# Kernel tuning notes

Hardware: AMD Instinct MI355X
Metric: run time of the kernel (lower is better)

## Reference

```python
import math
import jax, jax.numpy as jnp
import numpy as np

B, T, C = 2, 2048, 2048
NQ, NKV, H = 16, 4, 128
EPS = 1e-6
ROPE_BASE = 5.0e6


def setup_inputs() -> dict:
    key = jax.random.key(0)
    ks = jax.random.split(key, 6)
    x = jax.random.normal(ks[0], (B, T, C), dtype=jnp.float32)
    s = 0.02
    Wq = jax.random.normal(ks[1], (C, NQ * H), dtype=jnp.float32) * s
    Wk = jax.random.normal(ks[2], (C, NKV * H), dtype=jnp.float32) * s
    Wv = jax.random.normal(ks[3], (C, NKV * H), dtype=jnp.float32) * s
    Wo = jax.random.normal(ks[4], (NQ * H, C), dtype=jnp.float32) * s
    q_norm_w = jnp.ones((H,), dtype=jnp.float32)
    k_norm_w = jnp.ones((H,), dtype=jnp.float32)
    # RoPE tables (seq_start = 0)
    inv_freq = 1.0 / (ROPE_BASE ** (jnp.arange(0, H, 2, dtype=jnp.float32) / H))
    t = jnp.arange(T, dtype=jnp.float32)
    freqs = jnp.einsum('i,j->ij', t, inv_freq)          # [T, H/2]
    emb = jnp.concatenate([freqs, freqs], axis=-1)       # [T, H]
    cos = jnp.cos(emb)
    sin = jnp.sin(emb)
    # additive causal mask (finite large negative to stay nan-free)
    causal = jnp.tril(jnp.ones((T, T), dtype=bool))
    attn_mask = jnp.where(causal, 0.0, -1e9).astype(jnp.float32)
    return {"x": x, "Wq": Wq, "Wk": Wk, "Wv": Wv, "Wo": Wo,
            "q_norm_w": q_norm_w, "k_norm_w": k_norm_w,
            "cos": cos, "sin": sin, "attn_mask": attn_mask}


def _rms_norm(x, w):
    # x: [..., H]
    var = jnp.mean(x * x, axis=-1, keepdims=True)
    return w * (x * jax.lax.rsqrt(var + EPS))


def _rotate_half(x):
    x1, x2 = jnp.split(x, 2, axis=-1)
    return jnp.concatenate([-x2, x1], axis=-1)


def reference(x, Wq, Wk, Wv, Wo, q_norm_w, k_norm_w, cos, sin, attn_mask):
    q = (x @ Wq).reshape(B, T, NQ, H)
    k = (x @ Wk).reshape(B, T, NKV, H)
    v = (x @ Wv).reshape(B, T, NKV, H)
    q = _rms_norm(q, q_norm_w)
    k = _rms_norm(k, k_norm_w)
    c = cos[None, :, None, :]  # [1,T,1,H]
    s = sin[None, :, None, :]
    q = q * c + _rotate_half(q) * s
    k = k * c + _rotate_half(k) * s
    rep = NQ // NKV
    k = jnp.repeat(k, rep, axis=2)  # [B,T,NQ,H]
    v = jnp.repeat(v, rep, axis=2)
    scores = jnp.einsum('bihd,bjhd->bhij', q, k) / math.sqrt(H)
    scores = scores + attn_mask[None, None, :, :]
    probs = jax.nn.softmax(scores, axis=-1)
    ctx = jnp.einsum('bhij,bjhd->bihd', probs, v).reshape(B, T, NQ * H)
    return ctx @ Wo
```

## Files before the change

### kernel.cpp

```cpp
#include <hip/hip_runtime.h>
#include <hip/hip_bf16.h>

#define B_   2
#define T_   2048
#define C_   2048
#define NQ_  16
#define NKV_ 4
#define H_   128

using bf16x8 = __attribute__((ext_vector_type(8))) short;
using f32x4  = __attribute__((ext_vector_type(4))) float;

__device__ __forceinline__ unsigned short f2bf(float f) {
    __hip_bfloat16 h = __float2bfloat16(f);
    union { __hip_bfloat16 h; unsigned short s; } c;
    c.h = h;
    return c.s;
}
__device__ __forceinline__ float bf2f(unsigned short s) {
    return __uint_as_float(((unsigned)s) << 16);
}
__device__ __forceinline__ bf16x8 pack8(float4 f0, float4 f1) {
    bf16x8 r;
    r[0] = (short)f2bf(f0.x); r[1] = (short)f2bf(f0.y);
    r[2] = (short)f2bf(f0.z); r[3] = (short)f2bf(f0.w);
    r[4] = (short)f2bf(f1.x); r[5] = (short)f2bf(f1.y);
    r[6] = (short)f2bf(f1.z); r[7] = (short)f2bf(f1.w);
    return r;
}

#define MFMA16(a, b, c) __builtin_amdgcn_mfma_f32_16x16x32_bf16(a, b, c, 0, 0, 0)

__device__ __forceinline__ void gl_lds16(const void* g, void* l) {
    __builtin_amdgcn_global_load_lds(
        (const __attribute__((address_space(1))) void*)g,
        (__attribute__((address_space(3))) void*)l, 16, 0, 0);
}

__global__ void cvt_bf16(const float* __restrict__ src,
                         unsigned short* __restrict__ dst) {
    const int i = (blockIdx.x * 256 + threadIdx.x) * 8;
    const float4 a = *(const float4*)(src + i);
    const float4 b = *(const float4*)(src + i + 4);
    *(bf16x8*)(dst + i) = pack8(a, b);
}

__global__ void transpose_cvt(const float* __restrict__ src,
                              unsigned short* __restrict__ dst,
                              int R, int Cc) {
    const int tc = Cc >> 6;
    const int r0 = (blockIdx.x / tc) * 64;
    const int c0 = (blockIdx.x % tc) * 64;
    __shared__ unsigned short Tl[64 * 65];
    const int tid = threadIdx.x;
#pragma unroll
    for (int it = 0; it < 16; ++it) {
        const int idx = it * 256 + tid;
        const int r = idx >> 6, c = idx & 63;
        Tl[c * 65 + r] = f2bf(src[(size_t)(r0 + r) * Cc + c0 + c]);
    }
    __syncthreads();
#pragma unroll
    for (int it = 0; it < 16; ++it) {
        const int idx = it * 256 + tid;
        const int c = idx >> 6, r = idx & 63;
        dst[(size_t)(c0 + c) * R + r0 + r] = Tl[c * 65 + r];
    }
}

template <bool OUT_F32>
__global__ __launch_bounds__(256, 2) void gemm_bt(
    const unsigned short* __restrict__ Ab,
    const unsigned short* __restrict__ Bt,
    void* __restrict__ Cqv,
    unsigned short* __restrict__ Ck,
    unsigned short* __restrict__ Cv,
    int M, int N, int K, int fused) {
    const int ntn = N >> 7;
    const int cpx = gridDim.x >> 3;
    const int wg  = (blockIdx.x & 7) * cpx + (blockIdx.x >> 3);
    const int tm  = wg / ntn;
    const int tn  = wg % ntn;

    const int tid  = threadIdx.x;
    const int wv   = tid >> 6;
    const int lane = tid & 63;
    const int col  = lane & 15;
    const int quad = lane >> 4;
    const int wm   = (wv & 1) * 64;
    const int wn   = (wv >> 1) * 64;

    __shared__ unsigned short Al[3][128 * 32];
    __shared__ unsigned short Bl[3][128 * 32];

    f32x4 acc[4][4];
#pragma unroll
    for (int mt = 0; mt < 4; ++mt)
#pragma unroll
        for (int nt = 0; nt < 4; ++nt) acc[mt][nt] = (f32x4){0.f, 0.f, 0.f, 0.f};

    const int rsl = lane >> 2;
    const int gsw = ((lane & 3) ^ (rsl & 3)) << 3;
    const int row0 = wv * 32 + rsl;
    const int row1 = row0 + 16;
    const size_t aoff0 = (size_t)(tm * 128 + row0) * K + gsw;
    const size_t aoff1 = (size_t)(tm * 128 + row1) * K + gsw;
    const size_t boff0 = (size_t)(tn * 128 + row0) * K + gsw;
    const size_t boff1 = (size_t)(tn * 128 + row1) * K + gsw;
    const int ld0 = (wv * 32) * 32;
    const int ld1 = (wv * 32 + 16) * 32;

    auto stage = [&](int buf, int k0) {
        gl_lds16(Ab + aoff0 + k0, &Al[buf][ld0]);
        gl_lds16(Ab + aoff1 + k0, &Al[buf][ld1]);
        gl_lds16(Bt + boff0 + k0, &Bl[buf][ld0]);
        gl_lds16(Bt + boff1 + k0, &Bl[buf][ld1]);
    };

    const int swq = (quad ^ (col & 3)) << 3;
    const int NT  = K >> 5;

    stage(0, 0);
    stage(1, 32);
    asm volatile("s_waitcnt vmcnt(4)" ::: "memory");
    __builtin_amdgcn_sched_barrier(0);
    __builtin_amdgcn_s_barrier();

    int cur = 0;
    for (int t = 0; t < NT; ++t) {
        if (t + 2 < NT) {
            int b2 = cur + 2; if (b2 >= 3) b2 -= 3;
            stage(b2, (t + 2) << 5);
        }

        bf16x8 af[4], bfv[4];
#pragma unroll
        for (int q = 0; q < 4; ++q) {
            af[q]  = *(const bf16x8*)(&Al[cur][(wm + q * 16 + col) * 32 + swq]);
            bfv[q] = *(const bf16x8*)(&Bl[cur][(wn + q * 16 + col) * 32 + swq]);
        }
#pragma unroll
        for (int mt = 0; mt < 4; ++mt)
#pragma unroll
            for (int nt = 0; nt < 4; ++nt)
                acc[mt][nt] = MFMA16(af[mt], bfv[nt], acc[mt][nt]);

        asm volatile("s_waitcnt vmcnt(4)" ::: "memory");
        __builtin_amdgcn_sched_barrier(0);
        __builtin_amdgcn_s_barrier();
        ++cur; if (cur >= 3) cur -= 3;
    }

    const int nb = tn * 128;
    if constexpr (OUT_F32) {
        float* Co = (float*)Cqv;
#pragma unroll
        for (int mt = 0; mt < 4; ++mt)
#pragma unroll
            for (int nt = 0; nt < 4; ++nt)
#pragma unroll
                for (int r = 0; r < 4; ++r) {
                    const int row = tm * 128 + wm + mt * 16 + quad * 4 + r;
                    const int cc  = nb + wn + nt * 16 + col;
                    Co[(size_t)row * N + cc] = acc[mt][nt][r];
                }
    } else {
        unsigned short* Cb;
        int ldc, nc0;
        if (!fused)         { Cb = (unsigned short*)Cqv; ldc = N;    nc0 = nb;        }
        else if (nb < 2048) { Cb = (unsigned short*)Cqv; ldc = 2048; nc0 = nb;        }
        else if (nb < 2560) { Cb = Ck;                   ldc = 512;  nc0 = nb - 2048; }
        else                { Cb = Cv;                   ldc = 512;  nc0 = nb - 2560; }
#pragma unroll
        for (int mt = 0; mt < 4; ++mt)
#pragma unroll
            for (int nt = 0; nt < 4; ++nt)
#pragma unroll
                for (int r = 0; r < 4; ++r) {
                    const int row = tm * 128 + wm + mt * 16 + quad * 4 + r;
                    const int cc  = nc0 + wn + nt * 16 + col;
                    Cb[(size_t)row * ldc + cc] = f2bf(acc[mt][nt][r]);
                }
    }
}

__global__ void norm_rope(unsigned short* __restrict__ buf,
                          const float* __restrict__ w,
                          const float* __restrict__ cosb,
                          const float* __restrict__ sinb,
                          int nheads, float oscale) {
    const int idx = blockIdx.x;
    const int h   = idx % nheads;
    const int bt  = idx / nheads;
    const int t   = bt % T_;
    unsigned short* row = buf + ((size_t)bt * nheads + h) * H_;
    const int l = threadIdx.x;

    const float x0 = bf2f(row[l]);
    const float x1 = bf2f(row[l + 64]);
    float ss = x0 * x0 + x1 * x1;
#pragma unroll
    for (int off = 32; off; off >>= 1) ss += __shfl_xor(ss, off);
    const float r = rsqrtf(ss * (1.0f / 128.0f) + 1e-6f) * oscale;

    const float n0 = x0 * r * w[l];
    const float n1 = x1 * r * w[l + 64];
    const float c0 = cosb[t * H_ + l];
    const float c1 = cosb[t * H_ + l + 64];
    const float s0 = sinb[t * H_ + l];
    const float s1 = sinb[t * H_ + l + 64];

    row[l]      = f2bf(n0 * c0 - n1 * s0);
    row[l + 64] = f2bf(n1 * c1 + n0 * s1);
}

__global__ __launch_bounds__(512, 2) void flash_attn(
    const unsigned short* __restrict__ qbuf,
    const unsigned short* __restrict__ kbuf,
    const unsigned short* __restrict__ vbuf,
    unsigned short* __restrict__ ctx) {
    const int blk = blockIdx.x;
    const int p   = blk & 7;
    const int h   = (blk >> 3) & 15;
    const int b   = blk >> 7;
    const int kvh = h >> 2;
    const int qtB = 15 - p;

    const int tid  = threadIdx.x;
    const int wave = tid >> 6;
    const int g    = wave >> 2;
    const int gw   = wave & 3;
    const int lane = tid & 63;
    const int col  = lane & 15;
    const int quad = lane >> 4;
    const int gtid = gw * 64 + lane;

    int w0 = (g ? qtB : p) * 128 + gw * 32;
    const int ph1 = 2 * p + 2;

    __shared__ __align__(16) unsigned char smem[76800];
    unsigned short* Vg   = (unsigned short*)smem + g * 9216;
    unsigned short* Pw   = (unsigned short*)(smem + 36864) + wave * 2304;
    float*          alfw = (float*)(smem + 73728) + wave * 32;
    unsigned*       Vw   = (unsigned*)Vg;

    bf16x8 qf[2][4];
    auto loadQ = [&]() {
#pragma unroll
        for (int nt = 0; nt < 2; ++nt)
#pragma unroll
            for (int ks = 0; ks < 4; ++ks) {
                const size_t off =
                    ((size_t)(b * T_ + w0 + nt * 16 + col) * NQ_ + h) * H_ + ks * 32 + quad * 8;
                qf[nt][ks] = *(const bf16x8*)(qbuf + off);
            }
    };
    loadQ();

    f32x4 O[2][8];
#pragma unroll
    for (int pt = 0; pt < 2; ++pt)
#pragma unroll
        for (int dt = 0; dt < 8; ++dt) O[pt][dt] = (f32x4){0.f, 0.f, 0.f, 0.f};
    float m_run[2] = {-3.0e38f, -3.0e38f};
    float l_run[2] = {0.f, 0.f};

    bf16x8 kf[4][4];
    const unsigned short* kb = kbuf + ((size_t)(b * T_) * NKV_ + kvh) * H_;
    const int koff = col * (NKV_ * H_) + quad * 8;
    auto loadK = [&](int j0) {
#pragma unroll
        for (int mt = 0; mt < 4; ++mt) {
            const unsigned short* kr = kb + (size_t)((j0 + mt * 16) * (NKV_ * H_) + koff);
#pragma unroll
            for (int ks = 0; ks < 4; ++ks)
                kf[mt][ks] = *(const bf16x8*)(kr + ks * 32);
        }
    };

    uint4 va[4];
    const size_t kvstride = (size_t)NKV_ * H_;
    auto issueV = [&](int j0) {
#pragma unroll
        for (int it = 0; it < 2; ++it) {
            const int idx = it * 256 + gtid;
            const int kp  = idx & 31;
            const int dc  = idx >> 5;
            const size_t g0 = ((size_t)(b * T_ + j0 + 2 * kp) * NKV_ + kvh) * H_ + dc * 8;
            va[2 * it]     = *(const uint4*)(vbuf + g0);
            va[2 * it + 1] = *(const uint4*)(vbuf + g0 + kvstride);
        }
    };
    auto writeV = [&]() {
#pragma unroll
        for (int it = 0; it < 2; ++it) {
            const int idx = it * 256 + gtid;
            const int kp  = idx & 31;
            const int dc  = idx >> 5;
            const uint4 v0 = va[2 * it];
            const uint4 v1 = va[2 * it + 1];
            const int wb = dc * 288 + kp;
            Vw[wb + 0 * 36] = (v0.x & 0xFFFFu) | (v1.x << 16);
            Vw[wb + 1 * 36] = (v0.x >> 16)     | (v1.x & 0xFFFF0000u);
            Vw[wb + 2 * 36] = (v0.y & 0xFFFFu) | (v1.y << 16);
            Vw[wb + 3 * 36] = (v0.y >> 16)     | (v1.y & 0xFFFF0000u);
            Vw[wb + 4 * 36] = (v0.z & 0xFFFFu) | (v1.z << 16);
            Vw[wb + 5 * 36] = (v0.z >> 16)     | (v1.z & 0xFFFF0000u);
            Vw[wb + 6 * 36] = (v0.w & 0xFFFFu) | (v1.w << 16);
            Vw[wb + 7 * 36] = (v0.w >> 16)     | (v1.w & 0xFFFF0000u);
        }
    };

    auto storeOut = [&]() {
        if (quad == 0) {
            alfw[col]      = 1.0f / l_run[0];
            alfw[col + 16] = 1.0f / l_run[1];
        }
        const f32x4 i0 = *(const f32x4*)&alfw[quad * 4];
        const f32x4 i1 = *(const f32x4*)&alfw[quad * 4 + 16];
#pragma unroll
        for (int pt = 0; pt < 2; ++pt)
#pragma unroll
            for (int r = 0; r < 4; ++r) {
                const float inv = pt ? i1[r] : i0[r];
                const int ig = w0 + pt * 16 + quad * 4 + r;
                unsigned short* op = ctx + ((size_t)(b * T_ + ig) * NQ_ + h) * H_;
#pragma unroll
                for (int dt = 0; dt < 8; ++dt)
                    op[dt * 16 + col] = f2bf(O[pt][dt][r] * inv);
            }
    };

    auto chunk_of = [&](int i) { return g ? i : (i < ph1 ? i : i + 15 - 2 * p); };

    loadK(0);
    issueV(0);

    for (int i = 0; i < 17; ++i) {
        const int j0 = chunk_of(i) * 64;
        __syncthreads();
        writeV();
        __syncthreads();

        if (i + 1 < 17) issueV(chunk_of(i + 1) * 64);

        if (g == 0 && i == ph1) {
            storeOut();
#pragma unroll
            for (int pt = 0; pt < 2; ++pt)
#pragma unroll
                for (int dt = 0; dt < 8; ++dt) O[pt][dt] = (f32x4){0.f, 0.f, 0.f, 0.f};
            m_run[0] = m_run[1] = -3.0e38f;
            l_run[0] = l_run[1] = 0.f;
            w0 = qtB * 128 + gw * 32;
            loadQ();
        }

        const bool act = (j0 <= w0 + 31);

        f32x4 St[4][2];
        if (act) {
#pragma unroll
            for (int mt = 0; mt < 4; ++mt)
#pragma unroll
                for (int nt = 0; nt < 2; ++nt) St[mt][nt] = (f32x4){0.f, 0.f, 0.f, 0.f};
#pragma unroll
            for (int ks = 0; ks < 4; ++ks)
#pragma unroll
                for (int mt = 0; mt < 4; ++mt) {
                    St[mt][0] = MFMA16(kf[mt][ks], qf[0][ks], St[mt][0]);
                    St[mt][1] = MFMA16(kf[mt][ks], qf[1][ks], St[mt][1]);
                }
        }

        if (i + 1 < 17) loadK(chunk_of(i + 1) * 64);

        if (!act) continue;

        const bool needmask = (j0 + 63 > w0);
        if (needmask) {
            const int ig0 = w0 + col;
#pragma unroll
            for (int mt = 0; mt < 4; ++mt)
#pragma unroll
                for (int r = 0; r < 4; ++r) {
                    const int key = j0 + mt * 16 + quad * 4 + r;
                    if (key > ig0)      St[mt][0][r] = -3.0e38f;
                    if (key > ig0 + 16) St[mt][1][r] = -3.0e38f;
                }
        }

        float rm[2];
#pragma unroll
        for (int nt = 0; nt < 2; ++nt) {
            float m0 = fmaxf(fmaxf(St[0][nt][0], St[0][nt][1]),
                             fmaxf(St[0][nt][2], St[0][nt][3]));
#pragma unroll
            for (int mt = 1; mt < 4; ++mt)
                m0 = fmaxf(m0, fmaxf(fmaxf(St[mt][nt][0], St[mt][nt][1]),
                                     fmaxf(St[mt][nt][2], St[mt][nt][3])));
            m0 = fmaxf(m0, __shfl_xor(m0, 16));
            m0 = fmaxf(m0, __shfl_xor(m0, 32));
            rm[nt] = m0;
        }

        const int defer = __all((rm[0] <= m_run[0] + 8.0f) && (rm[1] <= m_run[1] + 8.0f));
        if (!defer) {
            const float mn0 = fmaxf(m_run[0], rm[0]);
            const float mn1 = fmaxf(m_run[1], rm[1]);
            const float al0 = exp2f(m_run[0] - mn0);
            const float al1 = exp2f(m_run[1] - mn1);
            m_run[0] = mn0; m_run[1] = mn1;
            l_run[0] *= al0; l_run[1] *= al1;
            if (quad == 0) { alfw[col] = al0; alfw[col + 16] = al1; }
        }

        float ls0 = 0.f, ls1 = 0.f;
#pragma unroll
        for (int mt = 0; mt < 4; ++mt) {
            const float p0 = exp2f(St[mt][0][0] - m_run[0]);
            const float p1 = exp2f(St[mt][0][1] - m_run[0]);
            const float p2 = exp2f(St[mt][0][2] - m_run[0]);
            const float p3 = exp2f(St[mt][0][3] - m_run[0]);
            ls0 += (p0 + p1) + (p2 + p3);
            *(uint2*)(Pw + col * 72 + mt * 16 + quad * 4) =
                make_uint2((unsigned)f2bf(p0) | ((unsigned)f2bf(p1) << 16),
                           (unsigned)f2bf(p2) | ((unsigned)f2bf(p3) << 16));
            const float q0 = exp2f(St[mt][1][0] - m_run[1]);
            const float q1 = exp2f(St[mt][1][1] - m_run[1]);
            const float q2 = exp2f(St[mt][1][2] - m_run[1]);
            const float q3 = exp2f(St[mt][1][3] - m_run[1]);
            ls1 += (q0 + q1) + (q2 + q3);
            *(uint2*)(Pw + (col + 16) * 72 + mt * 16 + quad * 4) =
                make_uint2((unsigned)f2bf(q0) | ((unsigned)f2bf(q1) << 16),
                           (unsigned)f2bf(q2) | ((unsigned)f2bf(q3) << 16));
        }
        ls0 += __shfl_xor(ls0, 16); ls0 += __shfl_xor(ls0, 32);
        ls1 += __shfl_xor(ls1, 16); ls1 += __shfl_xor(ls1, 32);
        l_run[0] += ls0; l_run[1] += ls1;

        if (!defer) {
            const f32x4 a0 = *(const f32x4*)&alfw[quad * 4];
            const f32x4 a1 = *(const f32x4*)&alfw[quad * 4 + 16];
#pragma unroll
            for (int dt = 0; dt < 8; ++dt)
#pragma unroll
                for (int r = 0; r < 4; ++r) { O[0][dt][r] *= a0[r]; O[1][dt][r] *= a1[r]; }
        }

#pragma unroll
        for (int ks = 0; ks < 2; ++ks) {
            const bf16x8 pa0 = *(const bf16x8*)(Pw + col * 72 + ks * 32 + quad * 8);
            const bf16x8 pa1 = *(const bf16x8*)(Pw + (col + 16) * 72 + ks * 32 + quad * 8);
#pragma unroll
            for (int dt = 0; dt < 8; ++dt) {
                const bf16x8 vf = *(const bf16x8*)(Vg + (dt * 16 + col) * 72 + ks * 32 + quad * 8);
                O[0][dt] = MFMA16(pa0, vf, O[0][dt]);
                O[1][dt] = MFMA16(pa1, vf, O[1][dt]);
            }
        }
    }

    __syncthreads();
    float* mlA = (float*)(smem + 74752);
    float* mlB = (float*)(smem + 75776);
    if (g == 0) {
        float* Of = (float*)smem + gw * 4096;
        float* ml = mlA + gw * 64;
        if (quad == 0) {
            ml[2 * col]            = m_run[0]; ml[2 * col + 1]        = l_run[0];
            ml[2 * (col + 16)]     = m_run[1]; ml[2 * (col + 16) + 1] = l_run[1];
        }
#pragma unroll
        for (int pt = 0; pt < 2; ++pt)
#pragma unroll
            for (int dt = 0; dt < 8; ++dt)
#pragma unroll
                for (int r = 0; r < 4; ++r)
                    Of[(pt * 16 + quad * 4 + r) * 128 + dt * 16 + col] = O[pt][dt][r];
    }
    __syncthreads();
    if (g == 1) {
        float* Of = (float*)smem + gw * 4096;
        float* mA = mlA + gw * 64;
        float* mB = mlB + gw * 64;
        if (quad == 0) {
            mB[2 * col]            = m_run[0]; mB[2 * col + 1]        = l_run[0];
            mB[2 * (col + 16)]     = m_run[1]; mB[2 * (col + 16) + 1] = l_run[1];
        }
#pragma unroll
        for (int pt = 0; pt < 2; ++pt)
#pragma unroll
            for (int r = 0; r < 4; ++r) {
                const int row = pt * 16 + quad * 4 + r;
                const float mBv = mB[2 * row], lBv = mB[2 * row + 1];
                const float mAv = mA[2 * row], lAv = mA[2 * row + 1];
                const float m  = fmaxf(mAv, mBv);
                const float aB = exp2f(mBv - m);
                const float aA = exp2f(mAv - m);
                const float inv = 1.0f / (lBv * aB + lAv * aA);
                const int ig = w0 + row;
                unsigned short* op = ctx + ((size_t)(b * T_ + ig) * NQ_ + h) * H_;
#pragma unroll
                for (int dt = 0; dt < 8; ++dt)
                    op[dt * 16 + col] =
                        f2bf((O[pt][dt][r] * aB + Of[row * 128 + dt * 16 + col] * aA) * inv);
            }
    }
}

extern "C" void kernel_launch(void* const* d_in, const int* in_sizes, int n_in,
                              void* d_out, int out_size, void* d_ws, size_t ws_size,
                              hipStream_t stream) {
    const float* x    = (const float*)d_in[0];
    const float* Wq   = (const float*)d_in[1];
    const float* Wk   = (const float*)d_in[2];
    const float* Wv   = (const float*)d_in[3];
    const float* Wo   = (const float*)d_in[4];
    const float* qnw  = (const float*)d_in[5];
    const float* knw  = (const float*)d_in[6];
    const float* cosb = (const float*)d_in[7];
    const float* sinb = (const float*)d_in[8];

    const int M = B_ * T_;
    unsigned short* ws  = (unsigned short*)d_ws;
    unsigned short* WqT = ws;
    unsigned short* WkT = WqT + (size_t)2048 * 2048;
    unsigned short* WvT = WkT + (size_t)512 * 2048;
    unsigned short* ctx = ws;
    unsigned short* q   = ws + (size_t)8388608;
    unsigned short* k   = ws + (size_t)16777216;
    unsigned short* v   = ws + (size_t)18874368;
    unsigned short* WoT = q;
    unsigned short* xbf = (unsigned short*)d_out;

    transpose_cvt<<<(2048 / 64) * (2048 / 64), 256, 0, stream>>>(Wq, WqT, 2048, 2048);
    transpose_cvt<<<(2048 / 64) * (512 / 64),  256, 0, stream>>>(Wk, WkT, 2048, 512);
    transpose_cvt<<<(2048 / 64) * (512 / 64),  256, 0, stream>>>(Wv, WvT, 2048, 512);
    cvt_bf16<<<(M * C_) / (256 * 8), 256, 0, stream>>>(x, xbf);

    gemm_bt<false><<<(M / 128) * (3072 / 128), 256, 0, stream>>>(
        xbf, WqT, (void*)q, k, v, M, 3072, C_, 1);

    norm_rope<<<M * NQ_, 64, 0, stream>>>(q, qnw, cosb, sinb, NQ_, 0.12751743f);
    norm_rope<<<M * NKV_, 64, 0, stream>>>(k, knw, cosb, sinb, NKV_, 1.0f);

    flash_attn<<<256, 512, 0, stream>>>(q, k, v, ctx);

    transpose_cvt<<<(2048 / 64) * (2048 / 64), 256, 0, stream>>>(Wo, WoT, 2048, 2048);
    gemm_bt<true><<<(M / 128) * (C_ / 128), 256, 0, stream>>>(
        ctx, WoT, d_out, nullptr, nullptr, M, C_, NQ_ * H_, 0);
}
```

Baseline: 370.2 us.

## Fuse RMS norm and RoPE into QKV GEMM epilogue

Removes the two separate norm_rope launches and applies RMS normalization and rotary embedding inside the QKV GEMM epilogue. Each 128-wide N tile is exactly one head, so row sums of squares are reduced with shuffles plus a small LDS exchange, and the rotate-half partner is read back from an LDS staging buffer. Launch bounds also move from 2 to 3 blocks per CU. This saves a round trip of Q/K through global memory and two kernel launches, at the cost of extra epilogue syncs, more register pressure, and an extra bf16 rounding of the partner value.

```diff
diff --git a/kernel.cpp b/kernel.cpp
--- a/kernel.cpp
+++ b/kernel.cpp
@@ -69,12 +69,16 @@
 }
 
 template <bool OUT_F32>
-__global__ __launch_bounds__(256, 2) void gemm_bt(
+__global__ __launch_bounds__(256, 3) void gemm_bt(
     const unsigned short* __restrict__ Ab,
     const unsigned short* __restrict__ Bt,
     void* __restrict__ Cqv,
     unsigned short* __restrict__ Ck,
     unsigned short* __restrict__ Cv,
+    const float* __restrict__ qnw,
+    const float* __restrict__ knw,
+    const float* __restrict__ cosb,
+    const float* __restrict__ sinb,
     int M, int N, int K, int fused) {
     const int ntn = N >> 7;
     const int cpx = gridDim.x >> 3;
@@ -90,8 +94,7 @@
     const int wm   = (wv & 1) * 64;
     const int wn   = (wv >> 1) * 64;
 
-    __shared__ unsigned short Al[3][128 * 32];
-    __shared__ unsigned short Bl[3][128 * 32];
+    __shared__ unsigned short gsm[24576];
 
     f32x4 acc[4][4];
 #pragma unroll
@@ -111,10 +114,10 @@
     const int ld1 = (wv * 32 + 16) * 32;
 
     auto stage = [&](int buf, int k0) {
-        gl_lds16(Ab + aoff0 + k0, &Al[buf][ld0]);
-        gl_lds16(Ab + aoff1 + k0, &Al[buf][ld1]);
-        gl_lds16(Bt + boff0 + k0, &Bl[buf][ld0]);
-        gl_lds16(Bt + boff1 + k0, &Bl[buf][ld1]);
+        gl_lds16(Ab + aoff0 + k0, gsm + buf * 4096 + ld0);
+        gl_lds16(Ab + aoff1 + k0, gsm + buf * 4096 + ld1);
+        gl_lds16(Bt + boff0 + k0, gsm + 12288 + buf * 4096 + ld0);
+        gl_lds16(Bt + boff1 + k0, gsm + 12288 + buf * 4096 + ld1);
     };
 
     const int swq = (quad ^ (col & 3)) << 3;
@@ -136,8 +139,8 @@
         bf16x8 af[4], bfv[4];
 #pragma unroll
         for (int q = 0; q < 4; ++q) {
-            af[q]  = *(const bf16x8*)(&Al[cur][(wm + q * 16 + col) * 32 + swq]);
-            bfv[q] = *(const bf16x8*)(&Bl[cur][(wn + q * 16 + col) * 32 + swq]);
+            af[q]  = *(const bf16x8*)(gsm + cur * 4096 + (wm + q * 16 + col) * 32 + swq);
+            bfv[q] = *(const bf16x8*)(gsm + 12288 + cur * 4096 + (wn + q * 16 + col) * 32 + swq);
         }
 #pragma unroll
         for (int mt = 0; mt < 4; ++mt)
@@ -171,47 +174,89 @@
         else if (nb < 2048) { Cb = (unsigned short*)Cqv; ldc = 2048; nc0 = nb;        }
         else if (nb < 2560) { Cb = Ck;                   ldc = 512;  nc0 = nb - 2048; }
         else                { Cb = Cv;                   ldc = 512;  nc0 = nb - 2560; }
-#pragma unroll
-        for (int mt = 0; mt < 4; ++mt)
-#pragma unroll
-            for (int nt = 0; nt < 4; ++nt)
+
+        if (fused && nb < 2560) {
+            const float osc = (nb < 2048) ? 0.12751743f : 1.0f;
+            const float* wn_ptr = (nb < 2048) ? qnw : knw;
+            unsigned short* nrm = gsm;
+            float* ssb = (float*)(gsm + 17408);
+
+            __syncthreads();
+
+            float ssp[4][4];
+#pragma unroll
+            for (int mt = 0; mt < 4; ++mt)
 #pragma unroll
                 for (int r = 0; r < 4; ++r) {
-                    const int row = tm * 128 + wm + mt * 16 + quad * 4 + r;
-                    const int cc  = nc0 + wn + nt * 16 + col;
-                    Cb[(size_t)row * ldc + cc] = f2bf(acc[mt][nt][r]);
+                    float s = acc[mt][0][r] * acc[mt][0][r] +
+                              acc[mt][1][r] * acc[mt][1][r] +
+                              acc[mt][2][r] * acc[mt][2][r] +
+                              acc[mt][3][r] * acc[mt][3][r];
+                    s += __shfl_xor(s, 1);
+                    s += __shfl_xor(s, 2);
+                    s += __shfl_xor(s, 4);
+                    s += __shfl_xor(s, 8);
+                    ssp[mt][r] = s;
                 }
-    }
-}
-
-__global__ void norm_rope(unsigned short* __restrict__ buf,
-                          const float* __restrict__ w,
-                          const float* __restrict__ cosb,
-                          const float* __restrict__ sinb,
-                          int nheads, float oscale) {
-    const int idx = blockIdx.x;
-    const int h   = idx % nheads;
-    const int bt  = idx / nheads;
-    const int t   = bt % T_;
-    unsigned short* row = buf + ((size_t)bt * nheads + h) * H_;
-    const int l = threadIdx.x;
-
-    const float x0 = bf2f(row[l]);
-    const float x1 = bf2f(row[l + 64]);
-    float ss = x0 * x0 + x1 * x1;
-#pragma unroll
-    for (int off = 32; off; off >>= 1) ss += __shfl_xor(ss, off);
-    const float r = rsqrtf(ss * (1.0f / 128.0f) + 1e-6f) * oscale;
-
-    const float n0 = x0 * r * w[l];
-    const float n1 = x1 * r * w[l + 64];
-    const float c0 = cosb[t * H_ + l];
-    const float c1 = cosb[t * H_ + l + 64];
-    const float s0 = sinb[t * H_ + l];
-    const float s1 = sinb[t * H_ + l + 64];
-
-    row[l]      = f2bf(n0 * c0 - n1 * s0);
-    row[l + 64] = f2bf(n1 * c1 + n0 * s1);
+            if (col == 0) {
+#pragma unroll
+                for (int mt = 0; mt < 4; ++mt)
+#pragma unroll
+                    for (int r = 0; r < 4; ++r)
+                        ssb[(wv >> 1) * 128 + wm + mt * 16 + quad * 4 + r] = ssp[mt][r];
+            }
+            __syncthreads();
+
+            float wld[4];
+#pragma unroll
+            for (int nt = 0; nt < 4; ++nt) wld[nt] = wn_ptr[wn + nt * 16 + col];
+#pragma unroll
+            for (int mt = 0; mt < 4; ++mt)
+#pragma unroll
+                for (int r = 0; r < 4; ++r) {
+                    const int rl = wm + mt * 16 + quad * 4 + r;
+                    const float ss = ssb[rl] + ssb[128 + rl];
+                    const float rinv = rsqrtf(ss * (1.0f / 128.0f) + 1e-6f) * osc;
+#pragma unroll
+                    for (int nt = 0; nt < 4; ++nt) {
+                        acc[mt][nt][r] *= rinv * wld[nt];
+                        nrm[rl * 132 + wn + nt * 16 + col] = f2bf(acc[mt][nt][r]);
+                    }
+                }
+            __syncthreads();
+
+#pragma unroll
+            for (int mt = 0; mt < 4; ++mt)
+#pragma unroll
+                for (int r = 0; r < 4; ++r) {
+                    const int rl = wm + mt * 16 + quad * 4 + r;
+                    const int grow = tm * 128 + rl;
+                    const float* cb = cosb + (size_t)(grow & 2047) * 128;
+                    const float* sb = sinb + (size_t)(grow & 2047) * 128;
+#pragma unroll
+                    for (int nt = 0; nt < 4; ++nt) {
+                        const int d = wn + nt * 16 + col;
+                        const float nd = acc[mt][nt][r];
+                        const float np = bf2f(nrm[rl * 132 + (d ^ 64)]);
+                        const float c = cb[d], s = sb[d];
+                        const float o = (wn == 0) ? nd * c - np * s
+                                                  : nd * c + np * s;
+                        Cb[(size_t)grow * ldc + nc0 + d] = f2bf(o);
+                    }
+                }
+        } else {
+#pragma unroll
+            for (int mt = 0; mt < 4; ++mt)
+#pragma unroll
+                for (int nt = 0; nt < 4; ++nt)
+#pragma unroll
+                    for (int r = 0; r < 4; ++r) {
+                        const int row = tm * 128 + wm + mt * 16 + quad * 4 + r;
+                        const int cc  = nc0 + wn + nt * 16 + col;
+                        Cb[(size_t)row * ldc + cc] = f2bf(acc[mt][nt][r]);
+                    }
+        }
+    }
 }
 
 __global__ __launch_bounds__(512, 2) void flash_attn(
@@ -540,14 +585,12 @@
     cvt_bf16<<<(M * C_) / (256 * 8), 256, 0, stream>>>(x, xbf);
 
     gemm_bt<false><<<(M / 128) * (3072 / 128), 256, 0, stream>>>(
-        xbf, WqT, (void*)q, k, v, M, 3072, C_, 1);
-
-    norm_rope<<<M * NQ_, 64, 0, stream>>>(q, qnw, cosb, sinb, NQ_, 0.12751743f);
-    norm_rope<<<M * NKV_, 64, 0, stream>>>(k, knw, cosb, sinb, NKV_, 1.0f);
+        xbf, WqT, (void*)q, k, v, qnw, knw, cosb, sinb, M, 3072, C_, 1);
 
     flash_attn<<<256, 512, 0, stream>>>(q, k, v, ctx);
 
     transpose_cvt<<<(2048 / 64) * (2048 / 64), 256, 0, stream>>>(Wo, WoT, 2048, 2048);
     gemm_bt<true><<<(M / 128) * (C_ / 128), 256, 0, stream>>>(
-        ctx, WoT, d_out, nullptr, nullptr, M, C_, NQ_ * H_, 0);
-}
+        ctx, WoT, d_out, nullptr, nullptr, nullptr, nullptr, nullptr, nullptr,
+        M, C_, NQ_ * H_, 0);
+}
```

Result: faster. 353.9 us (-4.4%).
